# Kernel optimization log

Hardware: AMD Instinct MI355X
Metric: run time of the kernel (lower is better)

## Reference

```python
import jax, jax.numpy as jnp
import numpy as np

EMBED = 1024
HEADS = 16
HDIM = 64
OUT = 1024
SCALE = HDIM ** (-0.5)


def setup_inputs() -> dict:
    key = jax.random.key(0)
    ks = jax.random.split(key, 12)
    B, L = 4, 1024
    k = jax.random.normal(ks[0], (B, L, EMBED), dtype=jnp.float32)
    q = jax.random.normal(ks[1], (B, L, EMBED), dtype=jnp.float32)
    v = jax.random.normal(ks[2], (B, L, EMBED), dtype=jnp.float32)
    # Linear params stored as [in, out]; scaled like torch default init
    lim = EMBED ** (-0.5)
    Wq = jax.random.uniform(ks[3], (EMBED, HEADS * HDIM), jnp.float32, -lim, lim)
    bq = jax.random.uniform(ks[4], (HEADS * HDIM,), jnp.float32, -lim, lim)
    Wk = jax.random.uniform(ks[5], (EMBED, HEADS * HDIM), jnp.float32, -lim, lim)
    Wv = jax.random.uniform(ks[6], (EMBED, HEADS * HDIM), jnp.float32, -lim, lim)
    limp = (HEADS * HDIM) ** (-0.5)
    Wp = jax.random.uniform(ks[7], (HEADS * HDIM, OUT), jnp.float32, -limp, limp)
    bp = jax.random.uniform(ks[8], (OUT,), jnp.float32, -limp, limp)
    attn_w = jax.random.uniform(ks[9], (2 * HDIM,), jnp.float32, -SCALE, SCALE)
    gamma = jnp.ones((OUT,), jnp.float32)
    beta = jnp.zeros((OUT,), jnp.float32)
    return {"k": k, "q": q, "v": v, "Wq": Wq, "bq": bq, "Wk": Wk, "Wv": Wv,
            "Wp": Wp, "bp": bp, "attn_w": attn_w, "gamma": gamma, "beta": beta}


def reference(k, q, v, Wq, bq, Wk, Wv, Wp, bp, attn_w, gamma, beta):
    B, Lq = q.shape[0], q.shape[1]
    Lk = k.shape[1]
    # QKV projections -> (b, len, heads, hdim)
    qh = (q @ Wq + bq).reshape(B, Lq, HEADS, HDIM)
    kh = (k @ Wk).reshape(B, Lk, HEADS, HDIM)
    vh = (v @ Wv).reshape(B, Lk, HEADS, HDIM)
    # mlp score: tanh(cat(q_i, k_j) . w) == tanh(q_i.w1 + k_j.w2); avoids
    # materializing the (b, q, k, n, 2d) padded tensor from the original.
    w1, w2 = attn_w[:HDIM], attn_w[HDIM:]
    sq = jnp.einsum('bind,d->bin', qh, w1)  # (b, q_len, heads)
    sk = jnp.einsum('bjnd,d->bjn', kh, w2)  # (b, k_len, heads)
    attn = jnp.tanh(sq[:, :, None, :] + sk[:, None, :, :])  # (b, i, j, n)
    attn = jax.nn.softmax(attn, axis=2)  # softmax over k_len (dim=2)
    out = jnp.einsum('bijn,bjnd->bind', attn, vh).reshape(B, Lq, HEADS * HDIM)
    out = out @ Wp + bp
    # LayerNorm eps=1e-6 (dropout is identity at p=0)
    mean = jnp.mean(out, axis=-1, keepdims=True)
    var = jnp.var(out, axis=-1, keepdims=True)
    out = (out - mean) / jnp.sqrt(var + 1e-6) * gamma + beta
    return out
```

## Files before the change

### kernel.cpp

```cpp
#include <hip/hip_runtime.h>
#include <math.h>

#define HEADS 16
#define HDIM  64
#define SEQ   1024
#define ROWS  4096
#define EMB   1024
#define MN    16

typedef _Float16 f16;
typedef __attribute__((ext_vector_type(4))) _Float16 f16x4;
typedef __attribute__((ext_vector_type(8))) _Float16 f16x8;
typedef __attribute__((ext_vector_type(4))) float f32x4;

__global__ __launch_bounds__(256) void fold_kernel(
    const float* __restrict__ Wq, const float* __restrict__ Wk,
    const float* __restrict__ bq, const float* __restrict__ attn_w,
    float* __restrict__ uq, float* __restrict__ uk, float* __restrict__ cq)
{
  int bid = blockIdx.x;
  if (bid < 128) {
    int idx = bid*256 + threadIdx.x;
    bool isQ = idx < 16384;
    int li = isQ ? idx : idx - 16384;
    int e = li >> 4, n = li & 15;
    const float* W = isQ ? Wq : Wk;
    const float* w = isQ ? attn_w : attn_w + HDIM;
    const float* wp = &W[(size_t)e*EMB + n*HDIM];
    float s = 0.f;
    #pragma unroll 16
    for (int d = 0; d < HDIM; ++d) s = fmaf(wp[d], w[d], s);
    (isQ ? uq : uk)[li] = s;
  } else if (threadIdx.x < 16) {
    int n = threadIdx.x;
    float s = 0.f;
    for (int d = 0; d < HDIM; ++d) s = fmaf(bq[n*HDIM+d], attn_w[d], s);
    cq[n] = s;
  }
}

__global__ __launch_bounds__(256) void sqsk2_kernel(
    const float* __restrict__ q, const float* __restrict__ k,
    const float* __restrict__ uq, const float* __restrict__ uk,
    const float* __restrict__ cq, float* __restrict__ sq, float* __restrict__ sk)
{
  __shared__ float rowbuf[8][EMB];
  __shared__ float part[16][8][17];
  int bid = blockIdx.x;
  bool isQ = bid < 512;
  int row0 = (isQ ? bid : bid - 512) * 8;
  const float* X = isQ ? q : k;
  const float* U = isQ ? uq : uk;
  int tid = threadIdx.x;
  #pragma unroll
  for (int p = 0; p < 8; ++p) {
    int fi = p*256 + tid;
    int r = fi >> 8, c4 = (fi & 255) * 4;
    *reinterpret_cast<float4*>(&rowbuf[r][c4]) =
        *reinterpret_cast<const float4*>(&X[(size_t)(row0 + r)*EMB + c4]);
  }
  __syncthreads();
  int n = tid & 15, ch = tid >> 4;
  float acc[8] = {0,0,0,0,0,0,0,0};
  #pragma unroll 4
  for (int e0 = 0; e0 < 64; ++e0) {
    int e = ch*64 + e0;
    float u = U[e*16 + n];
    #pragma unroll
    for (int r = 0; r < 8; ++r) acc[r] = fmaf(rowbuf[r][e], u, acc[r]);
  }
  #pragma unroll
  for (int r = 0; r < 8; ++r) part[ch][r][n] = acc[r];
  __syncthreads();
  if (tid < 128) {
    int r = tid >> 4, nn = tid & 15;
    float t = isQ ? cq[nn] : 0.f;
    #pragma unroll
    for (int c = 0; c < 16; ++c) t += part[c][r][nn];
    (isQ ? sq : sk)[(size_t)(row0 + r)*16 + nn] = t;
  }
}

__global__ __launch_bounds__(256) void nodes_kernel(const float* __restrict__ sq,
                                                    float* __restrict__ nodes)
{
  int bn = blockIdx.x;
  int b = bn >> 4, n = bn & 15;
  int tid = threadIdx.x;
  float mn = 1e30f, mx = -1e30f;
  #pragma unroll
  for (int s = 0; s < 4; ++s) {
    float v = sq[((size_t)(b*SEQ + tid + s*256))*16 + n];
    mn = fminf(mn, v); mx = fmaxf(mx, v);
  }
  __shared__ float smn[256], smx[256];
  smn[tid] = mn; smx[tid] = mx;
  __syncthreads();
  for (int off = 128; off > 0; off >>= 1) {
    if (tid < off) { smn[tid] = fminf(smn[tid], smn[tid+off]);
                     smx[tid] = fmaxf(smx[tid], smx[tid+off]); }
    __syncthreads();
  }
  if (tid < MN) {
    float c = 0.5f*(smn[0] + smx[0]);
    float r = fmaxf(0.5f*(smx[0] - smn[0]), 1e-4f);
    nodes[bn*MN + tid] = c + r * cosf(tid * (3.14159265358979323f / (MN-1)));
  }
}

__global__ __launch_bounds__(256) void ztrans_kernel(
    const float* __restrict__ v, const float* __restrict__ Wv,
    f16* __restrict__ vTh, f16* __restrict__ WvTh)
{
  __shared__ float tile[64][65];
  const int z = blockIdx.z;
  const int r0 = blockIdx.y * 64, c0 = blockIdx.x * 64;
  const int t = threadIdx.x, rr = t >> 4, c4 = (t & 15) * 4;
  const float* src = (z < 4) ? &v[(size_t)(z*SEQ + r0)*EMB + c0]
                             : &Wv[(size_t)r0*EMB + c0];
  #pragma unroll
  for (int i = 0; i < 4; ++i) {
    int row = rr + i * 16;
    float4 w = *reinterpret_cast<const float4*>(&src[(size_t)row*EMB + c4]);
    tile[row][c4] = w.x; tile[row][c4+1] = w.y;
    tile[row][c4+2] = w.z; tile[row][c4+3] = w.w;
  }
  __syncthreads();
  #pragma unroll
  for (int i = 0; i < 4; ++i) {
    int cc = rr + i * 16;
    f16x4 hh;
    #pragma unroll
    for (int jj = 0; jj < 4; ++jj) hh[jj] = (f16)tile[c4 + jj][cc];
    size_t o = (z < 4) ? ((size_t)(z*EMB + c0 + cc))*SEQ + r0 + c4
                       : ((size_t)(c0 + cc))*EMB + r0 + c4;
    *reinterpret_cast<f16x4*>(&((z < 4) ? vTh : WvTh)[o]) = hh;
  }
}

__global__ __launch_bounds__(256) void wmat_kernel(
    const float* __restrict__ sk, const float* __restrict__ nodes,
    f16* __restrict__ wh, float* __restrict__ Wn)
{
  __shared__ float sksh[256], nodesh[MN], Wnl[MN];
  const int qd = blockIdx.x, n = blockIdx.y, b = blockIdx.z;
  const int tid = threadIdx.x;
  const int j = qd*256 + tid;
  sksh[tid] = sk[((size_t)(b*SEQ + j))*16 + n];
  if (tid < MN) { nodesh[tid] = nodes[(b*16+n)*MN + tid]; Wnl[tid] = 0.f; }
  __syncthreads();
  const float skv = sksh[tid];
  const int lane = tid & 63;
  #pragma unroll 4
  for (int m = 0; m < MN; ++m) {
    float s = nodesh[m] + skv;
    float e2 = __expf(2.f * s);
    float th = 1.f - 2.f / (e2 + 1.f);
    float w = __expf(th);
    size_t row = (size_t)(b*256 + n*MN + m);
    wh[row*1024 + j] = (f16)w;
    float ws = w;
    #pragma unroll
    for (int off = 32; off > 0; off >>= 1) ws += __shfl_xor(ws, off);
    if (lane == 0) atomicAdd(&Wnl[m], ws);
  }
  __syncthreads();
  if (tid < MN) atomicAdd(&Wn[(b*16+n)*MN + tid], Wnl[tid]);
}

__global__ __launch_bounds__(256) void gemm1_f16(
    const f16* __restrict__ Ah, const f16* __restrict__ Bh,
    f16* __restrict__ Ch)
{
  __shared__ __align__(16) char lds[16384];
  const int tid = threadIdx.x;
  const int wid = tid >> 6, lane = tid & 63;
  int flat = blockIdx.y * 16 + blockIdx.x;
  int swz = (flat & 7) * 32 + (flat >> 3);
  const int bx = swz & 15, by = swz >> 4;
  const int z = by >> 2;
  const int grow = by * 64;
  const int bcol = bx * 64;
  const int wm = wid >> 1, wn = wid & 1;
  const int asel = lane >> 4, l15 = lane & 15;
  const int K = 1024, N = 1024;
  const f16* Bz_h = Bh + (size_t)z*EMB*SEQ;

  f32x4 acc[2][2];
  #pragma unroll
  for (int i = 0; i < 2; ++i)
    #pragma unroll
    for (int jx = 0; jx < 2; ++jx)
      acc[i][jx] = (f32x4){0.f, 0.f, 0.f, 0.f};

  for (int t = 0; t < 16; ++t) {
    const int k0 = t * 64;
    __syncthreads();
    #pragma unroll
    for (int r = 0; r < 4; ++r) {
      int ci = ((r & 1) << 8) + tid;
      int row = ci >> 3, kc = ci & 7;
      int kcg = kc ^ (row & 7);
      const f16* base = (r < 2) ? Ah : Bz_h;
      size_t roff = (r < 2) ? (size_t)(grow + row) : (size_t)(bcol + row);
      const char* src = (const char*)(base + roff * K + k0 + kcg * 8);
      char* dst = lds + (r * 256 + wid * 64) * 16;
      __builtin_amdgcn_global_load_lds(
          (const __attribute__((address_space(1))) unsigned int*)src,
          (__attribute__((address_space(3))) unsigned int*)dst, 16, 0, 0);
    }
    __syncthreads();
    #pragma unroll
    for (int kk = 0; kk < 2; ++kk) {
      f16x8 afh[2], bfh[2];
      #pragma unroll
      for (int mf = 0; mf < 2; ++mf) {
        int row = wm * 32 + mf * 16 + l15;
        int kcx = (kk * 4 + asel) ^ (row & 7);
        afh[mf] = *reinterpret_cast<const f16x8*>(lds + row * 128 + kcx * 16);
      }
      #pragma unroll
      for (int nf = 0; nf < 2; ++nf) {
        int col = wn * 32 + nf * 16 + l15;
        int kcx = (kk * 4 + asel) ^ (col & 7);
        bfh[nf] = *reinterpret_cast<const f16x8*>(lds + 8192 + col * 128 + kcx * 16);
      }
      #pragma unroll
      for (int mf = 0; mf < 2; ++mf)
        #pragma unroll
        for (int nf = 0; nf < 2; ++nf)
          acc[mf][nf] = __builtin_amdgcn_mfma_f32_16x16x32_f16(afh[mf], bfh[nf], acc[mf][nf], 0, 0, 0);
    }
  }
  const int crow0 = grow + wm * 32 + asel * 4;
  const int ccol0 = bcol + wn * 32 + l15;
  #pragma unroll
  for (int nf = 0; nf < 2; ++nf)
    #pragma unroll
    for (int mf = 0; mf < 2; ++mf)
      #pragma unroll
      for (int jx = 0; jx < 4; ++jx)
        Ch[(size_t)(crow0 + mf*16 + jx) * N + ccol0 + nf*16] = (f16)acc[mf][nf][jx];
}

__global__ __launch_bounds__(256) void coeff2_kernel(
    const float* __restrict__ sq, const float* __restrict__ nodes,
    const float* __restrict__ Wn, f16* __restrict__ csh, f16* __restrict__ csl)
{
  __shared__ float nsh[16][MN], wsh[16][MN];
  const int ic = blockIdx.x, b = blockIdx.y;
  const int tid = threadIdx.x;
  {
    int nn = tid >> 4, mm = tid & 15;
    nsh[nn][mm] = nodes[(b*16+nn)*MN + mm];
    wsh[nn][mm] = Wn[(b*16+nn)*MN + mm];
  }
  __syncthreads();
  const int il = tid >> 4, n = tid & 15;
  const int i = ic*16 + il;
  float s = sq[((size_t)(b*SEQ + i))*16 + n];
  float lam[MN];
  float den = 0.f;
  int ex = -1;
  #pragma unroll
  for (int m = 0; m < MN; ++m) {
    float diff = s - nsh[n][m];
    float wb = ((m == 0) | (m == MN-1)) ? 0.5f : 1.0f;
    wb = (m & 1) ? -wb : wb;
    if (diff == 0.f) ex = m;
    lam[m] = wb / diff;
    den = fmaf(lam[m], wsh[n][m], den);
  }
  float rden = 1024.f / den;
  f16* hp = &csh[((size_t)(b*SEQ + i))*256 + n*MN];
  f16* lp = &csl[((size_t)(b*SEQ + i))*256 + n*MN];
  #pragma unroll
  for (int m8 = 0; m8 < 2; ++m8) {
    f16x8 hv, lv;
    #pragma unroll
    for (int jj = 0; jj < 8; ++jj) {
      int m = m8*8 + jj;
      float c = (ex >= 0) ? ((m == ex) ? 1024.f/wsh[n][ex] : 0.f) : lam[m]*rden;
      f16 h = (f16)c;
      hv[jj] = h; lv[jj] = (f16)(c - (float)h);
    }
    *reinterpret_cast<f16x8*>(&hp[m8*8]) = hv;
    *reinterpret_cast<f16x8*>(&lp[m8*8]) = lv;
  }
}

__global__ __launch_bounds__(256) void ghprep_kernel(
    const f16* __restrict__ Ph, const f16* __restrict__ WvTh,
    const float* __restrict__ Wp, f16* __restrict__ Hsh, f16* __restrict__ Hsl)
{
  __shared__ float Gsh[MN][64];
  const int oc = blockIdx.x, n = blockIdx.y, b = blockIdx.z;
  const int bn = b*16 + n;
  const int tid = threadIdx.x;
  const int w = tid >> 6, lane = tid & 63;
  const int l15 = lane & 15, asel = lane >> 4;
  f32x4 acc = (f32x4){0.f,0.f,0.f,0.f};
  #pragma unroll 4
  for (int ks = 0; ks < 32; ++ks) {
    size_t bo = ((size_t)(n*64 + w*16 + l15))*1024 + ks*32 + asel*8;
    f16x8 bh = *reinterpret_cast<const f16x8*>(&WvTh[bo]);
    size_t ao = ((size_t)(bn*MN + l15))*1024 + ks*32 + asel*8;
    f16x8 ah = *reinterpret_cast<const f16x8*>(&Ph[ao]);
    acc = __builtin_amdgcn_mfma_f32_16x16x32_f16(ah, bh, acc, 0, 0, 0);
  }
  #pragma unroll
  for (int jx = 0; jx < 4; ++jx)
    Gsh[asel*4 + jx][w*16 + l15] = acc[jx];
  __syncthreads();
  const int o = oc*256 + tid;
  float a2[MN];
  #pragma unroll
  for (int m = 0; m < MN; ++m) a2[m] = 0.f;
  for (int d = 0; d < 64; ++d) {
    float wp = Wp[(size_t)(n*64 + d)*1024 + o];
    #pragma unroll
    for (int m = 0; m < MN; ++m) a2[m] = fmaf(wp, Gsh[m][d], a2[m]);
  }
  f16 hbuf[MN], lbuf[MN];
  #pragma unroll
  for (int m = 0; m < MN; ++m) {
    float vv = a2[m] * (1.f/1024.f);
    f16 h = (f16)vv;
    hbuf[m] = h; lbuf[m] = (f16)(vv - (float)h);
  }
  size_t base = ((size_t)(b*1024 + o))*256 + n*MN;
  #pragma unroll
  for (int m8 = 0; m8 < 2; ++m8) {
    *reinterpret_cast<f16x8*>(&Hsh[base + m8*8]) = *reinterpret_cast<f16x8*>(&hbuf[m8*8]);
    *reinterpret_cast<f16x8*>(&Hsl[base + m8*8]) = *reinterpret_cast<f16x8*>(&lbuf[m8*8]);
  }
}

__global__ __launch_bounds__(256) void gemm2_k(
    const f16* __restrict__ Ah, const f16* __restrict__ Al,
    const f16* __restrict__ Bh, const f16* __restrict__ Bl,
    const float* __restrict__ bias, float* __restrict__ Cf)
{
  __shared__ __align__(16) char lds[49152];
  const int tid = threadIdx.x;
  const int wid = tid >> 6, lane = tid & 63;
  int flat = (blockIdx.z * 8 + blockIdx.y) * 16 + blockIdx.x;
  int swz = (flat & 7) * 64 + (flat >> 3);
  const int bx = swz & 15;
  const int t2 = swz >> 4;
  const int by = t2 & 7, z = t2 >> 3;
  const int brow = by * 128;
  const int bcol = bx * 64;
  const int wm = wid >> 1, wn = wid & 1;
  const int asel = lane >> 4, l15 = lane & 15;
  const int K = 256, N = 1024, MZ = 1024;
  const f16* Az_h = Ah + (size_t)z*MZ*K;
  const f16* Az_l = Al + (size_t)z*MZ*K;
  const f16* Bz_h = Bh + (size_t)z*N*K;
  const f16* Bz_l = Bl + (size_t)z*N*K;

  f32x4 acc[4][2];
  #pragma unroll
  for (int i = 0; i < 4; ++i)
    #pragma unroll
    for (int jx = 0; jx < 2; ++jx)
      acc[i][jx] = (f32x4){0.f, 0.f, 0.f, 0.f};

  for (int t = 0; t < 4; ++t) {
    const int k0 = t * 64;
    __syncthreads();
    #pragma unroll
    for (int r = 0; r < 12; ++r) {
      const char* src;
      if (r < 8) {
        int ci = ((r & 3) << 8) + tid;
        int row = ci >> 3, kc = ci & 7;
        int kcg = kc ^ (row & 7);
        const f16* base = (r < 4) ? Az_h : Az_l;
        src = (const char*)(base + (size_t)(brow + row) * K + k0 + kcg * 8);
      } else {
        int ci = ((r & 1) << 8) + tid;
        int col = ci >> 3, kc = ci & 7;
        int kcg = kc ^ (col & 7);
        const f16* base = (r < 10) ? Bz_h : Bz_l;
        src = (const char*)(base + (size_t)(bcol + col) * K + k0 + kcg * 8);
      }
      char* dst = lds + (r * 256 + wid * 64) * 16;
      __builtin_amdgcn_global_load_lds(
          (const __attribute__((address_space(1))) unsigned int*)src,
          (__attribute__((address_space(3))) unsigned int*)dst, 16, 0, 0);
    }
    __syncthreads();
    #pragma unroll
    for (int kk = 0; kk < 2; ++kk) {
      f16x8 afh[4], afl[4], bfh[2], bfl[2];
      #pragma unroll
      for (int mf = 0; mf < 4; ++mf) {
        int row = wm * 64 + mf * 16 + l15;
        int kcx = (kk * 4 + asel) ^ (row & 7);
        int off = row * 128 + kcx * 16;
        afh[mf] = *reinterpret_cast<const f16x8*>(lds + off);
        afl[mf] = *reinterpret_cast<const f16x8*>(lds + 16384 + off);
      }
      #pragma unroll
      for (int nf = 0; nf < 2; ++nf) {
        int col = wn * 32 + nf * 16 + l15;
        int kcx = (kk * 4 + asel) ^ (col & 7);
        int off = col * 128 + kcx * 16;
        bfh[nf] = *reinterpret_cast<const f16x8*>(lds + 32768 + off);
        bfl[nf] = *reinterpret_cast<const f16x8*>(lds + 40960 + off);
      }
      #pragma unroll
      for (int mf = 0; mf < 4; ++mf)
        #pragma unroll
        for (int nf = 0; nf < 2; ++nf) {
          acc[mf][nf] = __builtin_amdgcn_mfma_f32_16x16x32_f16(afh[mf], bfh[nf], acc[mf][nf], 0, 0, 0);
          acc[mf][nf] = __builtin_amdgcn_mfma_f32_16x16x32_f16(afh[mf], bfl[nf], acc[mf][nf], 0, 0, 0);
          acc[mf][nf] = __builtin_amdgcn_mfma_f32_16x16x32_f16(afl[mf], bfh[nf], acc[mf][nf], 0, 0, 0);
        }
    }
  }
  const int crow0 = z*MZ + brow + wm * 64 + asel * 4;
  const int ccol0 = bcol + wn * 32 + l15;
  #pragma unroll
  for (int nf = 0; nf < 2; ++nf) {
    float bv = bias[ccol0 + nf * 16];
    #pragma unroll
    for (int mf = 0; mf < 4; ++mf)
      #pragma unroll
      for (int jx = 0; jx < 4; ++jx)
        Cf[(size_t)(crow0 + mf*16 + jx) * N + ccol0 + nf*16] = acc[mf][nf][jx] + bv;
  }
}

__global__ __launch_bounds__(256) void ln_kernel(
    float* __restrict__ out, const float* __restrict__ gamma,
    const float* __restrict__ beta)
{
  int row = blockIdx.x, tid = threadIdx.x;
  float4 x = *reinterpret_cast<float4*>(&out[(size_t)row*EMB + tid*4]);
  float sum = x.x + x.y + x.z + x.w;
  float ssq = x.x*x.x + x.y*x.y + x.z*x.z + x.w*x.w;
  #pragma unroll
  for (int off = 32; off > 0; off >>= 1) {
    sum += __shfl_down(sum, off);
    ssq += __shfl_down(ssq, off);
  }
  __shared__ float red[8];
  int wave = tid >> 6, lane = tid & 63;
  if (lane == 0) { red[wave] = sum; red[4+wave] = ssq; }
  __syncthreads();
  if (tid == 0) {
    float a = red[0]+red[1]+red[2]+red[3];
    float qq = red[4]+red[5]+red[6]+red[7];
    float mean = a * (1.f/EMB);
    float var  = qq * (1.f/EMB) - mean*mean;
    red[0] = mean;
    red[1] = 1.0f / sqrtf(var + 1e-6f);
  }
  __syncthreads();
  float mean = red[0], inv = red[1];
  float4 gv = *reinterpret_cast<const float4*>(&gamma[tid*4]);
  float4 bv = *reinterpret_cast<const float4*>(&beta[tid*4]);
  x.x = (x.x - mean)*inv*gv.x + bv.x;
  x.y = (x.y - mean)*inv*gv.y + bv.y;
  x.z = (x.z - mean)*inv*gv.z + bv.z;
  x.w = (x.w - mean)*inv*gv.w + bv.w;
  *reinterpret_cast<float4*>(&out[(size_t)row*EMB + tid*4]) = x;
}

extern "C" void kernel_launch(void* const* d_in, const int* in_sizes, int n_in,
                              void* d_out, int out_size, void* d_ws, size_t ws_size,
                              hipStream_t stream)
{
  const float* k   = (const float*)d_in[0];
  const float* q   = (const float*)d_in[1];
  const float* v   = (const float*)d_in[2];
  const float* Wq  = (const float*)d_in[3];
  const float* bq  = (const float*)d_in[4];
  const float* Wk  = (const float*)d_in[5];
  const float* Wv  = (const float*)d_in[6];
  const float* Wp  = (const float*)d_in[7];
  const float* bp  = (const float*)d_in[8];
  const float* aw  = (const float*)d_in[9];
  const float* gamma = (const float*)d_in[10];
  const float* beta  = (const float*)d_in[11];
  float* out = (float*)d_out;

  float* ws    = (float*)d_ws;
  float* uq    = ws;
  float* uk    = uq + 16384;
  float* cq    = uk + 16384;
  float* sq    = cq + 16;
  float* sk    = sq + 65536;
  float* nodes = sk + 65536;
  float* Wn    = nodes + 1024;
  const size_t MEG = 1048576;
  f16* f16b  = (f16*)(ws + 165904);
  f16* WvTh  = f16b;
  f16* vTh   = f16b + 1*MEG;
  f16* wh    = f16b + 5*MEG;
  f16* Ph    = f16b + 6*MEG;
  f16* csh   = f16b + 7*MEG;
  f16* csl   = f16b + 8*MEG;
  f16* Hsh   = f16b + 9*MEG;
  f16* Hsl   = f16b + 10*MEG;

  fold_kernel<<<129, 256, 0, stream>>>(Wq, Wk, bq, aw, uq, uk, cq);
  sqsk2_kernel<<<1024, 256, 0, stream>>>(q, k, uq, uk, cq, sq, sk);
  nodes_kernel<<<64, 256, 0, stream>>>(sq, nodes);
  ztrans_kernel<<<dim3(16,16,5), 256, 0, stream>>>(v, Wv, vTh, WvTh);
  hipMemsetAsync(Wn, 0, 1024*sizeof(float), stream);
  wmat_kernel<<<dim3(4,16,4), 256, 0, stream>>>(sk, nodes, wh, Wn);
  gemm1_f16<<<dim3(16,16), 256, 0, stream>>>(wh, vTh, Ph);
  coeff2_kernel<<<dim3(64,4), 256, 0, stream>>>(sq, nodes, Wn, csh, csl);
  ghprep_kernel<<<dim3(4,16,4), 256, 0, stream>>>(Ph, WvTh, Wp, Hsh, Hsl);
  gemm2_k<<<dim3(16,8,4), 256, 0, stream>>>(csh, csl, Hsh, Hsl, bp, out);
  ln_kernel<<<ROWS, 256, 0, stream>>>(out, gamma, beta);
}
```

Before: 196.1 us.

## Merge small kernels into horizontal fused launches and use one wave per LayerNorm row

```diff
diff --git a/kernel.cpp b/kernel.cpp
--- a/kernel.cpp
+++ b/kernel.cpp
@@ -1,10 +1,7 @@
 #include <hip/hip_runtime.h>
 #include <math.h>
 
-#define HEADS 16
-#define HDIM  64
 #define SEQ   1024
-#define ROWS  4096
 #define EMB   1024
 #define MN    16
 
@@ -13,29 +10,62 @@
 typedef __attribute__((ext_vector_type(8))) _Float16 f16x8;
 typedef __attribute__((ext_vector_type(4))) float f32x4;
 
-__global__ __launch_bounds__(256) void fold_kernel(
+__global__ __launch_bounds__(256) void prep_kernel(
     const float* __restrict__ Wq, const float* __restrict__ Wk,
-    const float* __restrict__ bq, const float* __restrict__ attn_w,
-    float* __restrict__ uq, float* __restrict__ uk, float* __restrict__ cq)
-{
-  int bid = blockIdx.x;
-  if (bid < 128) {
-    int idx = bid*256 + threadIdx.x;
+    const float* __restrict__ bq, const float* __restrict__ aw,
+    const float* __restrict__ v, const float* __restrict__ Wv,
+    float* __restrict__ uq, float* __restrict__ uk,
+    float* __restrict__ cq, float* __restrict__ Wn,
+    f16* __restrict__ vTh, f16* __restrict__ WvTh)
+{
+  __shared__ float tile[64][65];
+  const int t = blockIdx.x, tid = threadIdx.x;
+  if (t < 128) {
+    int idx = t*256 + tid;
     bool isQ = idx < 16384;
     int li = isQ ? idx : idx - 16384;
     int e = li >> 4, n = li & 15;
     const float* W = isQ ? Wq : Wk;
-    const float* w = isQ ? attn_w : attn_w + HDIM;
-    const float* wp = &W[(size_t)e*EMB + n*HDIM];
+    const float* w = isQ ? aw : aw + 64;
+    const float* wp = &W[(size_t)e*EMB + n*64];
     float s = 0.f;
     #pragma unroll 16
-    for (int d = 0; d < HDIM; ++d) s = fmaf(wp[d], w[d], s);
+    for (int d = 0; d < 64; ++d) s = fmaf(wp[d], w[d], s);
     (isQ ? uq : uk)[li] = s;
-  } else if (threadIdx.x < 16) {
-    int n = threadIdx.x;
-    float s = 0.f;
-    for (int d = 0; d < HDIM; ++d) s = fmaf(bq[n*HDIM+d], attn_w[d], s);
-    cq[n] = s;
+  } else if (t < 1408) {
+    int tt = t - 128;
+    int z = tt >> 8;
+    int ty = (tt >> 4) & 15, tx = tt & 15;
+    int r0 = ty*64, c0 = tx*64;
+    const float* src = (z < 4) ? &v[(size_t)(z*SEQ + r0)*EMB + c0]
+                               : &Wv[(size_t)r0*EMB + c0];
+    int rr = tid >> 4, c4 = (tid & 15)*4;
+    #pragma unroll
+    for (int i = 0; i < 4; ++i) {
+      int row = rr + i*16;
+      float4 wv = *reinterpret_cast<const float4*>(&src[(size_t)row*EMB + c4]);
+      tile[row][c4] = wv.x; tile[row][c4+1] = wv.y;
+      tile[row][c4+2] = wv.z; tile[row][c4+3] = wv.w;
+    }
+    __syncthreads();
+    #pragma unroll
+    for (int i = 0; i < 4; ++i) {
+      int cc = rr + i*16;
+      f16x4 hh;
+      #pragma unroll
+      for (int jj = 0; jj < 4; ++jj) hh[jj] = (f16)tile[c4+jj][cc];
+      size_t o = (z < 4) ? ((size_t)(z*EMB + c0 + cc))*SEQ + r0 + c4
+                         : ((size_t)(c0 + cc))*EMB + r0 + c4;
+      *reinterpret_cast<f16x4*>(&((z < 4) ? vTh : WvTh)[o]) = hh;
+    }
+  } else if (t == 1408) {
+    if (tid < 16) {
+      float s = 0.f;
+      for (int d = 0; d < 64; ++d) s = fmaf(bq[tid*64+d], aw[d], s);
+      cq[tid] = s;
+    }
+  } else {
+    for (int u = tid; u < 1024; u += 256) Wn[u] = 0.f;
   }
 }
 
@@ -48,16 +78,16 @@
   __shared__ float part[16][8][17];
   int bid = blockIdx.x;
   bool isQ = bid < 512;
-  int row0 = (isQ ? bid : bid - 512) * 8;
+  int row0 = (isQ ? bid : bid - 512)*8;
   const float* X = isQ ? q : k;
   const float* U = isQ ? uq : uk;
   int tid = threadIdx.x;
   #pragma unroll
   for (int p = 0; p < 8; ++p) {
     int fi = p*256 + tid;
-    int r = fi >> 8, c4 = (fi & 255) * 4;
+    int r = fi >> 8, c4 = (fi & 255)*4;
     *reinterpret_cast<float4*>(&rowbuf[r][c4]) =
-        *reinterpret_cast<const float4*>(&X[(size_t)(row0 + r)*EMB + c4]);
+        *reinterpret_cast<const float4*>(&X[(size_t)(row0+r)*EMB + c4]);
   }
   __syncthreads();
   int n = tid & 15, ch = tid >> 4;
@@ -74,26 +104,27 @@
   __syncthreads();
   if (tid < 128) {
     int r = tid >> 4, nn = tid & 15;
-    float t = isQ ? cq[nn] : 0.f;
-    #pragma unroll
-    for (int c = 0; c < 16; ++c) t += part[c][r][nn];
-    (isQ ? sq : sk)[(size_t)(row0 + r)*16 + nn] = t;
-  }
-}
-
-__global__ __launch_bounds__(256) void nodes_kernel(const float* __restrict__ sq,
-                                                    float* __restrict__ nodes)
-{
-  int bn = blockIdx.x;
-  int b = bn >> 4, n = bn & 15;
-  int tid = threadIdx.x;
+    float s = isQ ? cq[nn] : 0.f;
+    #pragma unroll
+    for (int c = 0; c < 16; ++c) s += part[c][r][nn];
+    (isQ ? sq : sk)[(size_t)(row0+r)*16 + nn] = s;
+  }
+}
+
+__global__ __launch_bounds__(256) void wmatn_kernel(
+    const float* __restrict__ sq, const float* __restrict__ sk,
+    f16* __restrict__ wh, float* __restrict__ nodes, float* __restrict__ Wn)
+{
+  __shared__ float smn[256], smx[256];
+  __shared__ float nodesh[MN], Wnl[MN];
+  const int qd = blockIdx.x, n = blockIdx.y, b = blockIdx.z;
+  const int tid = threadIdx.x;
   float mn = 1e30f, mx = -1e30f;
   #pragma unroll
   for (int s = 0; s < 4; ++s) {
-    float v = sq[((size_t)(b*SEQ + tid + s*256))*16 + n];
-    mn = fminf(mn, v); mx = fmaxf(mx, v);
-  }
-  __shared__ float smn[256], smx[256];
+    float vv = sq[((size_t)(b*SEQ + tid + s*256))*16 + n];
+    mn = fminf(mn, vv); mx = fmaxf(mx, vv);
+  }
   smn[tid] = mn; smx[tid] = mx;
   __syncthreads();
   for (int off = 128; off > 0; off >>= 1) {
@@ -102,63 +133,24 @@
     __syncthreads();
   }
   if (tid < MN) {
-    float c = 0.5f*(smn[0] + smx[0]);
-    float r = fmaxf(0.5f*(smx[0] - smn[0]), 1e-4f);
-    nodes[bn*MN + tid] = c + r * cosf(tid * (3.14159265358979323f / (MN-1)));
-  }
-}
-
-__global__ __launch_bounds__(256) void ztrans_kernel(
-    const float* __restrict__ v, const float* __restrict__ Wv,
-    f16* __restrict__ vTh, f16* __restrict__ WvTh)
-{
-  __shared__ float tile[64][65];
-  const int z = blockIdx.z;
-  const int r0 = blockIdx.y * 64, c0 = blockIdx.x * 64;
-  const int t = threadIdx.x, rr = t >> 4, c4 = (t & 15) * 4;
-  const float* src = (z < 4) ? &v[(size_t)(z*SEQ + r0)*EMB + c0]
-                             : &Wv[(size_t)r0*EMB + c0];
-  #pragma unroll
-  for (int i = 0; i < 4; ++i) {
-    int row = rr + i * 16;
-    float4 w = *reinterpret_cast<const float4*>(&src[(size_t)row*EMB + c4]);
-    tile[row][c4] = w.x; tile[row][c4+1] = w.y;
-    tile[row][c4+2] = w.z; tile[row][c4+3] = w.w;
+    float c = 0.5f*(smn[0]+smx[0]);
+    float r = fmaxf(0.5f*(smx[0]-smn[0]), 1e-4f);
+    float nv = c + r*cosf(tid*(3.14159265358979323f/(MN-1)));
+    nodesh[tid] = nv;
+    Wnl[tid] = 0.f;
+    if (qd == 0) nodes[(b*16+n)*MN + tid] = nv;
   }
   __syncthreads();
-  #pragma unroll
-  for (int i = 0; i < 4; ++i) {
-    int cc = rr + i * 16;
-    f16x4 hh;
-    #pragma unroll
-    for (int jj = 0; jj < 4; ++jj) hh[jj] = (f16)tile[c4 + jj][cc];
-    size_t o = (z < 4) ? ((size_t)(z*EMB + c0 + cc))*SEQ + r0 + c4
-                       : ((size_t)(c0 + cc))*EMB + r0 + c4;
-    *reinterpret_cast<f16x4*>(&((z < 4) ? vTh : WvTh)[o]) = hh;
-  }
-}
-
-__global__ __launch_bounds__(256) void wmat_kernel(
-    const float* __restrict__ sk, const float* __restrict__ nodes,
-    f16* __restrict__ wh, float* __restrict__ Wn)
-{
-  __shared__ float sksh[256], nodesh[MN], Wnl[MN];
-  const int qd = blockIdx.x, n = blockIdx.y, b = blockIdx.z;
-  const int tid = threadIdx.x;
   const int j = qd*256 + tid;
-  sksh[tid] = sk[((size_t)(b*SEQ + j))*16 + n];
-  if (tid < MN) { nodesh[tid] = nodes[(b*16+n)*MN + tid]; Wnl[tid] = 0.f; }
-  __syncthreads();
-  const float skv = sksh[tid];
+  const float skv = sk[((size_t)(b*SEQ + j))*16 + n];
   const int lane = tid & 63;
   #pragma unroll 4
   for (int m = 0; m < MN; ++m) {
     float s = nodesh[m] + skv;
-    float e2 = __expf(2.f * s);
-    float th = 1.f - 2.f / (e2 + 1.f);
+    float e2 = __expf(2.f*s);
+    float th = 1.f - 2.f/(e2+1.f);
     float w = __expf(th);
-    size_t row = (size_t)(b*256 + n*MN + m);
-    wh[row*1024 + j] = (f16)w;
+    wh[(size_t)(b*256 + n*MN + m)*1024 + j] = (f16)w;
     float ws = w;
     #pragma unroll
     for (int off = 32; off > 0; off >>= 1) ws += __shfl_xor(ws, off);
@@ -168,124 +160,120 @@
   if (tid < MN) atomicAdd(&Wn[(b*16+n)*MN + tid], Wnl[tid]);
 }
 
-__global__ __launch_bounds__(256) void gemm1_f16(
-    const f16* __restrict__ Ah, const f16* __restrict__ Bh,
-    f16* __restrict__ Ch)
-{
-  __shared__ __align__(16) char lds[16384];
-  const int tid = threadIdx.x;
-  const int wid = tid >> 6, lane = tid & 63;
-  int flat = blockIdx.y * 16 + blockIdx.x;
-  int swz = (flat & 7) * 32 + (flat >> 3);
-  const int bx = swz & 15, by = swz >> 4;
-  const int z = by >> 2;
-  const int grow = by * 64;
-  const int bcol = bx * 64;
-  const int wm = wid >> 1, wn = wid & 1;
-  const int asel = lane >> 4, l15 = lane & 15;
-  const int K = 1024, N = 1024;
-  const f16* Bz_h = Bh + (size_t)z*EMB*SEQ;
-
-  f32x4 acc[2][2];
-  #pragma unroll
-  for (int i = 0; i < 2; ++i)
-    #pragma unroll
-    for (int jx = 0; jx < 2; ++jx)
-      acc[i][jx] = (f32x4){0.f, 0.f, 0.f, 0.f};
-
-  for (int t = 0; t < 16; ++t) {
-    const int k0 = t * 64;
-    __syncthreads();
-    #pragma unroll
-    for (int r = 0; r < 4; ++r) {
-      int ci = ((r & 1) << 8) + tid;
-      int row = ci >> 3, kc = ci & 7;
-      int kcg = kc ^ (row & 7);
-      const f16* base = (r < 2) ? Ah : Bz_h;
-      size_t roff = (r < 2) ? (size_t)(grow + row) : (size_t)(bcol + row);
-      const char* src = (const char*)(base + roff * K + k0 + kcg * 8);
-      char* dst = lds + (r * 256 + wid * 64) * 16;
-      __builtin_amdgcn_global_load_lds(
-          (const __attribute__((address_space(1))) unsigned int*)src,
-          (__attribute__((address_space(3))) unsigned int*)dst, 16, 0, 0);
-    }
-    __syncthreads();
-    #pragma unroll
-    for (int kk = 0; kk < 2; ++kk) {
-      f16x8 afh[2], bfh[2];
-      #pragma unroll
-      for (int mf = 0; mf < 2; ++mf) {
-        int row = wm * 32 + mf * 16 + l15;
-        int kcx = (kk * 4 + asel) ^ (row & 7);
-        afh[mf] = *reinterpret_cast<const f16x8*>(lds + row * 128 + kcx * 16);
+__global__ __launch_bounds__(256) void g1c_kernel(
+    const f16* __restrict__ wh, const f16* __restrict__ vTh,
+    f16* __restrict__ Ph,
+    const float* __restrict__ sq, const float* __restrict__ nodes,
+    const float* __restrict__ Wn, f16* __restrict__ csh, f16* __restrict__ csl)
+{
+  __shared__ __align__(16) char SMEM[16384];
+  const int t = blockIdx.x, tid = threadIdx.x;
+  if (t < 256) {
+    int swz = (t & 7)*32 + (t >> 3);
+    int bx = swz & 15, by = swz >> 4;
+    int z = by >> 2;
+    int grow = by*64, bcol = bx*64;
+    int wid = tid >> 6, lane = tid & 63;
+    int wm = wid >> 1, wn = wid & 1;
+    int asel = lane >> 4, l15 = lane & 15;
+    const f16* Bz = vTh + (size_t)z*EMB*SEQ;
+    char* lds = SMEM;
+    f32x4 acc[2][2];
+    #pragma unroll
+    for (int i = 0; i < 2; ++i)
+      #pragma unroll
+      for (int jx = 0; jx < 2; ++jx)
+        acc[i][jx] = (f32x4){0.f,0.f,0.f,0.f};
+    for (int kt = 0; kt < 16; ++kt) {
+      const int k0 = kt*64;
+      __syncthreads();
+      #pragma unroll
+      for (int r = 0; r < 4; ++r) {
+        int ci = ((r & 1) << 8) + tid;
+        int row = ci >> 3, kc = ci & 7;
+        int kcg = kc ^ (row & 7);
+        const f16* base = (r < 2) ? wh : Bz;
+        size_t roff = (r < 2) ? (size_t)(grow + row) : (size_t)(bcol + row);
+        const char* src = (const char*)(base + roff*1024 + k0 + kcg*8);
+        char* dst = lds + (r*256 + wid*64)*16;
+        __builtin_amdgcn_global_load_lds(
+            (const __attribute__((address_space(1))) unsigned int*)src,
+            (__attribute__((address_space(3))) unsigned int*)dst, 16, 0, 0);
       }
-      #pragma unroll
-      for (int nf = 0; nf < 2; ++nf) {
-        int col = wn * 32 + nf * 16 + l15;
-        int kcx = (kk * 4 + asel) ^ (col & 7);
-        bfh[nf] = *reinterpret_cast<const f16x8*>(lds + 8192 + col * 128 + kcx * 16);
+      __syncthreads();
+      #pragma unroll
+      for (int kk = 0; kk < 2; ++kk) {
+        f16x8 afh[2], bfh[2];
+        #pragma unroll
+        for (int mf = 0; mf < 2; ++mf) {
+          int row = wm*32 + mf*16 + l15;
+          int kcx = (kk*4 + asel) ^ (row & 7);
+          afh[mf] = *reinterpret_cast<const f16x8*>(lds + row*128 + kcx*16);
+        }
+        #pragma unroll
+        for (int nf = 0; nf < 2; ++nf) {
+          int col = wn*32 + nf*16 + l15;
+          int kcx = (kk*4 + asel) ^ (col & 7);
+          bfh[nf] = *reinterpret_cast<const f16x8*>(lds + 8192 + col*128 + kcx*16);
+        }
+        #pragma unroll
+        for (int mf = 0; mf < 2; ++mf)
+          #pragma unroll
+          for (int nf = 0; nf < 2; ++nf)
+            acc[mf][nf] = __builtin_amdgcn_mfma_f32_16x16x32_f16(afh[mf], bfh[nf], acc[mf][nf], 0, 0, 0);
       }
+    }
+    const int crow0 = grow + wm*32 + asel*4;
+    const int ccol0 = bcol + wn*32 + l15;
+    #pragma unroll
+    for (int nf = 0; nf < 2; ++nf)
       #pragma unroll
       for (int mf = 0; mf < 2; ++mf)
         #pragma unroll
-        for (int nf = 0; nf < 2; ++nf)
-          acc[mf][nf] = __builtin_amdgcn_mfma_f32_16x16x32_f16(afh[mf], bfh[nf], acc[mf][nf], 0, 0, 0);
-    }
-  }
-  const int crow0 = grow + wm * 32 + asel * 4;
-  const int ccol0 = bcol + wn * 32 + l15;
-  #pragma unroll
-  for (int nf = 0; nf < 2; ++nf)
-    #pragma unroll
-    for (int mf = 0; mf < 2; ++mf)
-      #pragma unroll
-      for (int jx = 0; jx < 4; ++jx)
-        Ch[(size_t)(crow0 + mf*16 + jx) * N + ccol0 + nf*16] = (f16)acc[mf][nf][jx];
-}
-
-__global__ __launch_bounds__(256) void coeff2_kernel(
-    const float* __restrict__ sq, const float* __restrict__ nodes,
-    const float* __restrict__ Wn, f16* __restrict__ csh, f16* __restrict__ csl)
-{
-  __shared__ float nsh[16][MN], wsh[16][MN];
-  const int ic = blockIdx.x, b = blockIdx.y;
-  const int tid = threadIdx.x;
-  {
-    int nn = tid >> 4, mm = tid & 15;
-    nsh[nn][mm] = nodes[(b*16+nn)*MN + mm];
-    wsh[nn][mm] = Wn[(b*16+nn)*MN + mm];
-  }
-  __syncthreads();
-  const int il = tid >> 4, n = tid & 15;
-  const int i = ic*16 + il;
-  float s = sq[((size_t)(b*SEQ + i))*16 + n];
-  float lam[MN];
-  float den = 0.f;
-  int ex = -1;
-  #pragma unroll
-  for (int m = 0; m < MN; ++m) {
-    float diff = s - nsh[n][m];
-    float wb = ((m == 0) | (m == MN-1)) ? 0.5f : 1.0f;
-    wb = (m & 1) ? -wb : wb;
-    if (diff == 0.f) ex = m;
-    lam[m] = wb / diff;
-    den = fmaf(lam[m], wsh[n][m], den);
-  }
-  float rden = 1024.f / den;
-  f16* hp = &csh[((size_t)(b*SEQ + i))*256 + n*MN];
-  f16* lp = &csl[((size_t)(b*SEQ + i))*256 + n*MN];
-  #pragma unroll
-  for (int m8 = 0; m8 < 2; ++m8) {
-    f16x8 hv, lv;
-    #pragma unroll
-    for (int jj = 0; jj < 8; ++jj) {
-      int m = m8*8 + jj;
-      float c = (ex >= 0) ? ((m == ex) ? 1024.f/wsh[n][ex] : 0.f) : lam[m]*rden;
-      f16 h = (f16)c;
-      hv[jj] = h; lv[jj] = (f16)(c - (float)h);
-    }
-    *reinterpret_cast<f16x8*>(&hp[m8*8]) = hv;
-    *reinterpret_cast<f16x8*>(&lp[m8*8]) = lv;
+        for (int jx = 0; jx < 4; ++jx)
+          Ph[(size_t)(crow0 + mf*16 + jx)*1024 + ccol0 + nf*16] = (f16)acc[mf][nf][jx];
+  } else {
+    int tc = t - 256;
+    int ic = tc & 63, b = tc >> 6;
+    float (*nsh)[MN] = (float(*)[MN])SMEM;
+    float (*wsh)[MN] = ((float(*)[MN])SMEM) + 16;
+    {
+      int nn = tid >> 4, mm = tid & 15;
+      nsh[nn][mm] = nodes[(b*16+nn)*MN + mm];
+      wsh[nn][mm] = Wn[(b*16+nn)*MN + mm];
+    }
+    __syncthreads();
+    int il = tid >> 4, n = tid & 15;
+    int i = ic*16 + il;
+    float s = sq[((size_t)(b*SEQ + i))*16 + n];
+    float lam[MN];
+    float den = 0.f;
+    int ex = -1;
+    #pragma unroll
+    for (int m = 0; m < MN; ++m) {
+      float diff = s - nsh[n][m];
+      float wb = ((m == 0) | (m == MN-1)) ? 0.5f : 1.0f;
+      wb = (m & 1) ? -wb : wb;
+      if (diff == 0.f) ex = m;
+      lam[m] = wb / diff;
+      den = fmaf(lam[m], wsh[n][m], den);
+    }
+    float rden = 1024.f / den;
+    f16* hp = &csh[((size_t)(b*SEQ + i))*256 + n*MN];
+    f16* lp = &csl[((size_t)(b*SEQ + i))*256 + n*MN];
+    #pragma unroll
+    for (int m8 = 0; m8 < 2; ++m8) {
+      f16x8 hv, lv;
+      #pragma unroll
+      for (int jj = 0; jj < 8; ++jj) {
+        int m = m8*8 + jj;
+        float c = (ex >= 0) ? ((m == ex) ? 1024.f/wsh[n][ex] : 0.f) : lam[m]*rden;
+        f16 h = (f16)c;
+        hv[jj] = h; lv[jj] = (f16)(c - (float)h);
+      }
+      *reinterpret_cast<f16x8*>(&hp[m8*8]) = hv;
+      *reinterpret_cast<f16x8*>(&lp[m8*8]) = lv;
+    }
   }
 }
 
@@ -437,36 +425,36 @@
     float* __restrict__ out, const float* __restrict__ gamma,
     const float* __restrict__ beta)
 {
-  int row = blockIdx.x, tid = threadIdx.x;
-  float4 x = *reinterpret_cast<float4*>(&out[(size_t)row*EMB + tid*4]);
-  float sum = x.x + x.y + x.z + x.w;
-  float ssq = x.x*x.x + x.y*x.y + x.z*x.z + x.w*x.w;
+  const int t = blockIdx.x, tid = threadIdx.x;
+  int wid = tid >> 6, lane = tid & 63;
+  int row = t*4 + wid;
+  float4 x[4];
+  float sum = 0.f, ssq = 0.f;
+  #pragma unroll
+  for (int p = 0; p < 4; ++p) {
+    x[p] = *reinterpret_cast<float4*>(&out[(size_t)row*1024 + (p*64 + lane)*4]);
+    sum += x[p].x + x[p].y + x[p].z + x[p].w;
+    ssq += x[p].x*x[p].x + x[p].y*x[p].y + x[p].z*x[p].z + x[p].w*x[p].w;
+  }
   #pragma unroll
   for (int off = 32; off > 0; off >>= 1) {
-    sum += __shfl_down(sum, off);
-    ssq += __shfl_down(ssq, off);
-  }
-  __shared__ float red[8];
-  int wave = tid >> 6, lane = tid & 63;
-  if (lane == 0) { red[wave] = sum; red[4+wave] = ssq; }
-  __syncthreads();
-  if (tid == 0) {
-    float a = red[0]+red[1]+red[2]+red[3];
-    float qq = red[4]+red[5]+red[6]+red[7];
-    float mean = a * (1.f/EMB);
-    float var  = qq * (1.f/EMB) - mean*mean;
-    red[0] = mean;
-    red[1] = 1.0f / sqrtf(var + 1e-6f);
-  }
-  __syncthreads();
-  float mean = red[0], inv = red[1];
-  float4 gv = *reinterpret_cast<const float4*>(&gamma[tid*4]);
-  float4 bv = *reinterpret_cast<const float4*>(&beta[tid*4]);
-  x.x = (x.x - mean)*inv*gv.x + bv.x;
-  x.y = (x.y - mean)*inv*gv.y + bv.y;
-  x.z = (x.z - mean)*inv*gv.z + bv.z;
-  x.w = (x.w - mean)*inv*gv.w + bv.w;
-  *reinterpret_cast<float4*>(&out[(size_t)row*EMB + tid*4]) = x;
+    sum += __shfl_xor(sum, off);
+    ssq += __shfl_xor(ssq, off);
+  }
+  float mean = sum * (1.f/1024.f);
+  float var  = ssq * (1.f/1024.f) - mean*mean;
+  float inv  = 1.0f / sqrtf(var + 1e-6f);
+  #pragma unroll
+  for (int p = 0; p < 4; ++p) {
+    float4 gv = *reinterpret_cast<const float4*>(&gamma[(p*64 + lane)*4]);
+    float4 bv = *reinterpret_cast<const float4*>(&beta[(p*64 + lane)*4]);
+    float4 y;
+    y.x = (x[p].x - mean)*inv*gv.x + bv.x;
+    y.y = (x[p].y - mean)*inv*gv.y + bv.y;
+    y.z = (x[p].z - mean)*inv*gv.z + bv.z;
+    y.w = (x[p].w - mean)*inv*gv.w + bv.w;
+    *reinterpret_cast<float4*>(&out[(size_t)row*1024 + (p*64 + lane)*4]) = y;
+  }
 }
 
 extern "C" void kernel_launch(void* const* d_in, const int* in_sizes, int n_in,
@@ -496,25 +484,22 @@
   float* nodes = sk + 65536;
   float* Wn    = nodes + 1024;
   const size_t MEG = 1048576;
-  f16* f16b  = (f16*)(ws + 165904);
-  f16* WvTh  = f16b;
-  f16* vTh   = f16b + 1*MEG;
-  f16* wh    = f16b + 5*MEG;
-  f16* Ph    = f16b + 6*MEG;
-  f16* csh   = f16b + 7*MEG;
-  f16* csl   = f16b + 8*MEG;
-  f16* Hsh   = f16b + 9*MEG;
-  f16* Hsl   = f16b + 10*MEG;
-
-  fold_kernel<<<129, 256, 0, stream>>>(Wq, Wk, bq, aw, uq, uk, cq);
+  f16* f16b = (f16*)(ws + 165904);
+  f16* WvTh = f16b;
+  f16* vTh  = f16b + 1*MEG;
+  f16* wh   = f16b + 5*MEG;
+  f16* Ph   = f16b + 6*MEG;
+  f16* csh  = f16b + 7*MEG;
+  f16* csl  = f16b + 8*MEG;
+  f16* Hsh  = f16b + 9*MEG;
+  f16* Hsl  = f16b + 10*MEG;
+
+  prep_kernel<<<1410, 256, 0, stream>>>(Wq, Wk, bq, aw, v, Wv,
+                                        uq, uk, cq, Wn, vTh, WvTh);
   sqsk2_kernel<<<1024, 256, 0, stream>>>(q, k, uq, uk, cq, sq, sk);
-  nodes_kernel<<<64, 256, 0, stream>>>(sq, nodes);
-  ztrans_kernel<<<dim3(16,16,5), 256, 0, stream>>>(v, Wv, vTh, WvTh);
-  hipMemsetAsync(Wn, 0, 1024*sizeof(float), stream);
-  wmat_kernel<<<dim3(4,16,4), 256, 0, stream>>>(sk, nodes, wh, Wn);
-  gemm1_f16<<<dim3(16,16), 256, 0, stream>>>(wh, vTh, Ph);
-  coeff2_kernel<<<dim3(64,4), 256, 0, stream>>>(sq, nodes, Wn, csh, csl);
+  wmatn_kernel<<<dim3(4,16,4), 256, 0, stream>>>(sq, sk, wh, nodes, Wn);
+  g1c_kernel<<<512, 256, 0, stream>>>(wh, vTh, Ph, sq, nodes, Wn, csh, csl);
   ghprep_kernel<<<dim3(4,16,4), 256, 0, stream>>>(Ph, WvTh, Wp, Hsh, Hsl);
   gemm2_k<<<dim3(16,8,4), 256, 0, stream>>>(csh, csl, Hsh, Hsl, bp, out);
-  ln_kernel<<<ROWS, 256, 0, stream>>>(out, gamma, beta);
-}
+  ln_kernel<<<1024, 256, 0, stream>>>(out, gamma, beta);
+}
```

After: 183.2 us. -6.6%, faster.
